# Optimization experiments

Hardware: AMD Instinct MI355X
Metric: run time of the kernel (lower is better)

Reference implementation:

```python
import jax, jax.numpy as jnp
import numpy as np

B = 4096
P_HID = 1024
H_HID = 512
MAX_P = 128
MAX_HE = MAX_P // 3  # 42
TAU = 1.0
EPS = 1e-20


def setup_inputs() -> dict:
    key = jax.random.key(0)
    ks = jax.random.split(key, 12)
    s_p = 1.0 / np.sqrt(P_HID)
    s_h = 1.0 / np.sqrt(H_HID)
    # gumbel noise: g = -log(-log(U))
    u_p = jax.random.uniform(ks[3], (B, MAX_P, 2), minval=EPS, maxval=1.0)
    u_h = jax.random.uniform(ks[4], (B, MAX_HE, 2), minval=EPS, maxval=1.0)
    return {
        "particle_h": jax.random.normal(ks[0], (B, P_HID), jnp.float32),
        "edge_h": jax.random.normal(ks[1], (B, H_HID), jnp.float32),
        "hyperedge_h": jax.random.normal(ks[2], (B, H_HID), jnp.float32),
        "g_p": -jnp.log(-jnp.log(u_p)),
        "g_h": -jnp.log(-jnp.log(u_h)),
        "W1_p": jax.random.normal(ks[5], (P_HID, P_HID), jnp.float32) * s_p,
        "b1_p": jnp.zeros((P_HID,), jnp.float32),
        "W2_p": jax.random.normal(ks[6], (P_HID, MAX_P), jnp.float32) * s_p,
        "b2_p": jnp.zeros((MAX_P,), jnp.float32),
        "W1_h": jax.random.normal(ks[7], (H_HID, H_HID), jnp.float32) * s_h,
        "b1_h": jnp.zeros((H_HID,), jnp.float32),
        "W2_h": jax.random.normal(ks[8], (H_HID, MAX_HE), jnp.float32) * s_h,
        "b2_h": jnp.zeros((MAX_HE,), jnp.float32),
    }


def _gumbel_hard_st(logits, g, tau):
    """F.gumbel_softmax(stack([l,-l],-1), tau, hard=True)[...,0] (straight-through)."""
    y = jax.nn.softmax((jnp.stack([logits, -logits], axis=-1) + g) / tau, axis=-1)
    y0 = y[..., 0]
    hard0 = (y0 > y[..., 1]).astype(y0.dtype)
    return hard0 + y0 - jax.lax.stop_gradient(y0)


def _mlp(x, W1, b1, W2, b2):
    return jax.nn.gelu(x @ W1 + b1, approximate=False) @ W2 + b2


def reference(particle_h, edge_h, hyperedge_h, g_p, g_h,
              W1_p, b1_p, W2_p, b2_p, W1_h, b1_h, W2_h, b2_h):
    particle_logits = _mlp(particle_h, W1_p, b1_p, W2_p, b2_p)      # [B, MAX_P]
    particle_mask = _gumbel_hard_st(particle_logits, g_p, TAU)      # [B, MAX_P]
    n_particles = particle_mask.sum(axis=-1).astype(jnp.int32)      # [B]

    # Ragged edge lists as a fixed padded buffer: all C(MAX_P,2) lexicographic
    # pairs (same order as torch.combinations); pair (i,j), i<j, is valid for
    # batch b iff j < n_particles[b].
    ii, jj = jnp.triu_indices(MAX_P, k=1)
    edge_index = jnp.stack([ii, jj]).astype(jnp.int32)              # [2, E_max]
    edge_valid = jj[None, :] < n_particles[:, None]                 # [B, E_max] bool

    hyperedge_logits = _mlp(hyperedge_h, W1_h, b1_h, W2_h, b2_h)    # [B, MAX_HE]
    hyperedge_mask = _gumbel_hard_st(hyperedge_logits, g_h, TAU)
    n_hyperedges = hyperedge_mask.sum(axis=-1).astype(jnp.int32)

    return (particle_mask, n_particles, edge_index, edge_valid,
            hyperedge_mask, n_hyperedges)
```

## Files before the change

### kernel.cpp

```cpp
#include <hip/hip_runtime.h>
#include <hip/hip_bf16.h>
#include <math.h>

typedef __bf16 bf16_t;
typedef bf16_t bf16x8 __attribute__((ext_vector_type(8)));
typedef bf16_t bf16x4 __attribute__((ext_vector_type(4)));
typedef float f32x4 __attribute__((ext_vector_type(4)));
typedef unsigned int u32;

#define B_SZ 4096
#define P_HID 1024
#define H_HID 512
#define MAX_P 128
#define MAX_HE 42
#define HE_PAD 64
#define E_MAX 8128
#define E_MAX4 2032

__device__ __forceinline__ void async_cp16(const bf16_t* g, bf16_t* l) {
    __builtin_amdgcn_global_load_lds(
        (const __attribute__((address_space(1))) u32*)g,
        (__attribute__((address_space(3))) u32*)l, 16, 0, 0);
}

__device__ __forceinline__ float gelu_exact(float v) {
    return 0.5f * v * (1.f + erff(v * 0.70710678118654752f));
}

template<int BM, int BN, int MODE>
__global__ __launch_bounds__(256, 2) void gemm_sp(
    const bf16_t* __restrict__ Ahi, const bf16_t* __restrict__ Alo,
    const bf16_t* __restrict__ BThi, const bf16_t* __restrict__ BTlo,
    const float* __restrict__ bias,
    float* __restrict__ Cf, bf16_t* __restrict__ Chi, bf16_t* __restrict__ Clo,
    int M, int N, int K, int kchunk)
{
    constexpr int MT = BM / 32;
    constexpr int NT = BN / 32;
    constexpr int OPS_A = BM / 16;
    constexpr int OPS_B = BN / 16;
    constexpr int NOPS = 2 * OPS_A + 2 * OPS_B;

    __shared__ __align__(16) bf16_t smem[(2 * BM + 2 * BN) * 32];
    bf16_t* const As0 = smem;
    bf16_t* const As1 = smem + BM * 32;
    bf16_t* const Bs0 = smem + 2 * BM * 32;
    bf16_t* const Bs1 = smem + 2 * BM * 32 + BN * 32;

    const int tid  = threadIdx.x;
    const int lane = tid & 63;
    const int wid  = tid >> 6;
    const int wm   = wid & 1;
    const int wn   = wid >> 1;
    const int bm   = blockIdx.y * BM;
    const int bn   = blockIdx.x * BN;
    const int k0   = blockIdx.z * kchunk;

    const int srow = lane >> 2;
    const int scol = (lane & 3) * 8;

    f32x4 acc[MT][NT];
#pragma unroll
    for (int i = 0; i < MT; ++i)
#pragma unroll
        for (int j = 0; j < NT; ++j)
            acc[i][j] = (f32x4){0.f, 0.f, 0.f, 0.f};

    const bf16_t* const gA0 = Ahi  + (size_t)bm * K;
    const bf16_t* const gA1 = Alo  + (size_t)bm * K;
    const bf16_t* const gB0 = BThi + (size_t)bn * K;
    const bf16_t* const gB1 = BTlo + (size_t)bn * K;

    const int fr = lane & 15;
    const int fq = lane >> 4;

    for (int kt = k0; kt < k0 + kchunk; kt += 32) {
        __syncthreads();
#pragma unroll
        for (int o = 0; o < NOPS; ++o) {
            if ((o & 3) != wid) continue;
            const bf16_t* gsrc;
            bf16_t* lbase;
            int q;
            if (o < OPS_A)               { q = o;                 gsrc = gA0; lbase = As0; }
            else if (o < 2 * OPS_A)      { q = o - OPS_A;         gsrc = gA1; lbase = As1; }
            else if (o < 2 * OPS_A + OPS_B) { q = o - 2 * OPS_A;  gsrc = gB0; lbase = Bs0; }
            else                         { q = o - 2 * OPS_A - OPS_B; gsrc = gB1; lbase = Bs1; }
            async_cp16(gsrc + (size_t)(q * 16 + srow) * K + kt + scol,
                       lbase + q * 16 * 32);
        }
        __syncthreads();

        bf16x8 ah[MT], al[MT], bh[NT], bl[NT];
#pragma unroll
        for (int i = 0; i < MT; ++i) {
            const int row = wm * (BM / 2) + i * 16 + fr;
            ah[i] = *(const bf16x8*)(As0 + row * 32 + fq * 8);
            al[i] = *(const bf16x8*)(As1 + row * 32 + fq * 8);
        }
#pragma unroll
        for (int j = 0; j < NT; ++j) {
            const int row = wn * (BN / 2) + j * 16 + fr;
            bh[j] = *(const bf16x8*)(Bs0 + row * 32 + fq * 8);
            bl[j] = *(const bf16x8*)(Bs1 + row * 32 + fq * 8);
        }
#pragma unroll
        for (int i = 0; i < MT; ++i)
#pragma unroll
            for (int j = 0; j < NT; ++j) {
                acc[i][j] = __builtin_amdgcn_mfma_f32_16x16x32_bf16(ah[i], bh[j], acc[i][j], 0, 0, 0);
                acc[i][j] = __builtin_amdgcn_mfma_f32_16x16x32_bf16(ah[i], bl[j], acc[i][j], 0, 0, 0);
                acc[i][j] = __builtin_amdgcn_mfma_f32_16x16x32_bf16(al[i], bh[j], acc[i][j], 0, 0, 0);
            }
    }

#pragma unroll
    for (int i = 0; i < MT; ++i)
#pragma unroll
        for (int j = 0; j < NT; ++j) {
            const int col  = bn + wn * (BN / 2) + j * 16 + fr;
            const int row0 = bm + wm * (BM / 2) + i * 16 + fq * 4;
            if (MODE == 0) {
                const float bj = bias[col];
#pragma unroll
                for (int r = 0; r < 4; ++r) {
                    float v = gelu_exact(acc[i][j][r] + bj);
                    bf16_t h = (bf16_t)v;
                    bf16_t l = (bf16_t)(v - (float)h);
                    const size_t off = (size_t)(row0 + r) * N + col;
                    Chi[off] = h;
                    Clo[off] = l;
                }
            } else {
#pragma unroll
                for (int r = 0; r < 4; ++r)
                    atomicAdd(&Cf[(size_t)(row0 + r) * N + col], acc[i][j][r]);
            }
        }
}

__global__ __launch_bounds__(256) void split_rows(
    const float* __restrict__ x, bf16_t* __restrict__ hi, bf16_t* __restrict__ lo, int n4)
{
    int i = blockIdx.x * 256 + threadIdx.x;
    if (i >= n4) return;
    float4 v = ((const float4*)x)[i];
    float vv[4] = {v.x, v.y, v.z, v.w};
    bf16x4 h, l;
#pragma unroll
    for (int r = 0; r < 4; ++r) {
        bf16_t hh = (bf16_t)vv[r];
        h[r] = hh;
        l[r] = (bf16_t)(vv[r] - (float)hh);
    }
    ((bf16x4*)hi)[i] = h;
    ((bf16x4*)lo)[i] = l;
}

__global__ __launch_bounds__(256) void wsplit_t(
    const float* __restrict__ W, bf16_t* __restrict__ Thi, bf16_t* __restrict__ Tlo,
    int K, int N)
{
    __shared__ float t[32][33];
    const int n0 = blockIdx.x * 32, k0 = blockIdx.y * 32;
    const int tx = threadIdx.x & 31, ty = threadIdx.x >> 5;
    for (int r = ty; r < 32; r += 8) {
        const int n = n0 + tx;
        t[r][tx] = (n < N) ? W[(size_t)(k0 + r) * N + n] : 0.f;
    }
    __syncthreads();
    for (int r = ty; r < 32; r += 8) {
        const float x = t[tx][r];
        bf16_t h = (bf16_t)x;
        bf16_t l = (bf16_t)(x - (float)h);
        const size_t off = (size_t)(n0 + r) * K + k0 + tx;
        Thi[off] = h;
        Tlo[off] = l;
    }
}

__global__ __launch_bounds__(256) void init_logits(
    const float* __restrict__ b2p, const float* __restrict__ b2h,
    float* __restrict__ logp, float* __restrict__ logh)
{
    const int i = blockIdx.x * 256 + threadIdx.x;
    const int NP = B_SZ * MAX_P;
    if (i < NP) {
        logp[i] = b2p[i & (MAX_P - 1)];
    } else {
        const int r = i - NP;
        if (r < B_SZ * HE_PAD) {
            const int c = r & (HE_PAD - 1);
            logh[r] = (c < MAX_HE) ? b2h[c] : 0.f;
        }
    }
}

__global__ __launch_bounds__(64) void mask_count(
    const float* __restrict__ logits, const float* __restrict__ g,
    float* __restrict__ out_mask, float* __restrict__ out_n,
    int* __restrict__ ws_n, int L, int ls)
{
    const int b = blockIdx.x;
    const int t = threadIdx.x;
    float cnt = 0.f;
    for (int i = t; i < L; i += 64) {
        const float l  = logits[(size_t)b * ls + i];
        const float g0 = g[((size_t)b * L + i) * 2 + 0];
        const float g1 = g[((size_t)b * L + i) * 2 + 1];
        const float hard = ((l + g0) > (g1 - l)) ? 1.f : 0.f;
        out_mask[(size_t)b * L + i] = hard;
        cnt += hard;
    }
#pragma unroll
    for (int off = 32; off > 0; off >>= 1) cnt += __shfl_down(cnt, off, 64);
    if (t == 0) {
        out_n[b] = cnt;
        if (ws_n) ws_n[b] = (int)cnt;
    }
}

__device__ __forceinline__ int tri_off(int i) { return (i * (255 - i)) >> 1; }

__global__ __launch_bounds__(256) void edge_index_kernel(
    float* __restrict__ out_ei, int* __restrict__ ws_jj)
{
    int e = blockIdx.x * 256 + threadIdx.x;
    if (e >= E_MAX) return;
    int i = (int)((255.0 - sqrt(65025.0 - 8.0 * (double)e)) * 0.5);
    if (i < 0) i = 0;
    if (i > 126) i = 126;
    while (i > 0 && tri_off(i) > e) --i;
    while (i < 126 && tri_off(i + 1) <= e) ++i;
    int j = i + 1 + (e - tri_off(i));
    out_ei[e] = (float)i;
    out_ei[E_MAX + e] = (float)j;
    ws_jj[e] = j;
}

__global__ __launch_bounds__(256) void edge_valid_kernel(
    const int* __restrict__ ws_jj, const int* __restrict__ ws_n,
    float* __restrict__ out, int total4)
{
    int idx = blockIdx.x * 256 + threadIdx.x;
    if (idx >= total4) return;
    int b = idx / E_MAX4;
    int q = idx - b * E_MAX4;
    int4 j4 = ((const int4*)ws_jj)[q];
    int n = ws_n[b];
    float4 v;
    v.x = (j4.x < n) ? 1.f : 0.f;
    v.y = (j4.y < n) ? 1.f : 0.f;
    v.z = (j4.z < n) ? 1.f : 0.f;
    v.w = (j4.w < n) ? 1.f : 0.f;
    ((float4*)out)[idx] = v;
}

extern "C" void kernel_launch(void* const* d_in, const int* in_sizes, int n_in,
                              void* d_out, int out_size, void* d_ws, size_t ws_size,
                              hipStream_t stream)
{
    const float* particle_h  = (const float*)d_in[0];
    const float* hyperedge_h = (const float*)d_in[2];
    const float* g_p  = (const float*)d_in[3];
    const float* g_h  = (const float*)d_in[4];
    const float* W1_p = (const float*)d_in[5];
    const float* b1_p = (const float*)d_in[6];
    const float* W2_p = (const float*)d_in[7];
    const float* b2_p = (const float*)d_in[8];
    const float* W1_h = (const float*)d_in[9];
    const float* b1_h = (const float*)d_in[10];
    const float* W2_h = (const float*)d_in[11];
    const float* b2_h = (const float*)d_in[12];

    float* out = (float*)d_out;
    float* out_pmask = out;
    float* out_np    = out_pmask + (size_t)B_SZ * MAX_P;
    float* out_ei    = out_np + B_SZ;
    float* out_ev    = out_ei + 2 * E_MAX;
    float* out_hmask = out_ev + (size_t)B_SZ * E_MAX;
    float* out_nh    = out_hmask + (size_t)B_SZ * MAX_HE;

    char* w = (char*)d_ws;
    bf16_t* pA_hi  = (bf16_t*)w;                    w += (size_t)B_SZ * P_HID * 2;
    bf16_t* pA_lo  = (bf16_t*)w;                    w += (size_t)B_SZ * P_HID * 2;
    bf16_t* hA_hi  = (bf16_t*)w;                    w += (size_t)B_SZ * H_HID * 2;
    bf16_t* hA_lo  = (bf16_t*)w;                    w += (size_t)B_SZ * H_HID * 2;
    bf16_t* hidp_hi = (bf16_t*)w;                   w += (size_t)B_SZ * P_HID * 2;
    bf16_t* hidp_lo = (bf16_t*)w;                   w += (size_t)B_SZ * P_HID * 2;
    bf16_t* hidh_hi = (bf16_t*)w;                   w += (size_t)B_SZ * H_HID * 2;
    bf16_t* hidh_lo = (bf16_t*)w;                   w += (size_t)B_SZ * H_HID * 2;
    bf16_t* W1pT_hi = (bf16_t*)w;                   w += (size_t)P_HID * P_HID * 2;
    bf16_t* W1pT_lo = (bf16_t*)w;                   w += (size_t)P_HID * P_HID * 2;
    bf16_t* W2pT_hi = (bf16_t*)w;                   w += (size_t)MAX_P * P_HID * 2;
    bf16_t* W2pT_lo = (bf16_t*)w;                   w += (size_t)MAX_P * P_HID * 2;
    bf16_t* W1hT_hi = (bf16_t*)w;                   w += (size_t)H_HID * H_HID * 2;
    bf16_t* W1hT_lo = (bf16_t*)w;                   w += (size_t)H_HID * H_HID * 2;
    bf16_t* W2hT_hi = (bf16_t*)w;                   w += (size_t)HE_PAD * H_HID * 2;
    bf16_t* W2hT_lo = (bf16_t*)w;                   w += (size_t)HE_PAD * H_HID * 2;
    float*  log_p   = (float*)w;                    w += (size_t)B_SZ * MAX_P * 4;
    float*  log_h   = (float*)w;                    w += (size_t)B_SZ * HE_PAD * 4;
    int*    ws_np   = (int*)w;                      w += B_SZ * 4;
    int*    ws_jj   = (int*)w;

    split_rows<<<(B_SZ * P_HID / 4 + 255) / 256, 256, 0, stream>>>(
        particle_h, pA_hi, pA_lo, B_SZ * P_HID / 4);
    split_rows<<<(B_SZ * H_HID / 4 + 255) / 256, 256, 0, stream>>>(
        hyperedge_h, hA_hi, hA_lo, B_SZ * H_HID / 4);
    wsplit_t<<<dim3(P_HID / 32, P_HID / 32), 256, 0, stream>>>(W1_p, W1pT_hi, W1pT_lo, P_HID, P_HID);
    wsplit_t<<<dim3(MAX_P / 32, P_HID / 32), 256, 0, stream>>>(W2_p, W2pT_hi, W2pT_lo, P_HID, MAX_P);
    wsplit_t<<<dim3(H_HID / 32, H_HID / 32), 256, 0, stream>>>(W1_h, W1hT_hi, W1hT_lo, H_HID, H_HID);
    wsplit_t<<<dim3(HE_PAD / 32, H_HID / 32), 256, 0, stream>>>(W2_h, W2hT_hi, W2hT_lo, H_HID, MAX_HE);
    init_logits<<<(B_SZ * (MAX_P + HE_PAD) + 255) / 256, 256, 0, stream>>>(
        b2_p, b2_h, log_p, log_h);

    gemm_sp<64, 128, 0><<<dim3(P_HID / 128, B_SZ / 64, 1), 256, 0, stream>>>(
        pA_hi, pA_lo, W1pT_hi, W1pT_lo, b1_p, nullptr, hidp_hi, hidp_lo,
        B_SZ, P_HID, P_HID, P_HID);
    gemm_sp<64, 128, 1><<<dim3(1, B_SZ / 64, 4), 256, 0, stream>>>(
        hidp_hi, hidp_lo, W2pT_hi, W2pT_lo, nullptr, log_p, nullptr, nullptr,
        B_SZ, MAX_P, P_HID, P_HID / 4);
    mask_count<<<B_SZ, 64, 0, stream>>>(log_p, g_p, out_pmask, out_np, ws_np, MAX_P, MAX_P);

    gemm_sp<64, 64, 0><<<dim3(H_HID / 64, B_SZ / 64, 1), 256, 0, stream>>>(
        hA_hi, hA_lo, W1hT_hi, W1hT_lo, b1_h, nullptr, hidh_hi, hidh_lo,
        B_SZ, H_HID, H_HID, H_HID);
    gemm_sp<64, 64, 1><<<dim3(1, B_SZ / 64, 4), 256, 0, stream>>>(
        hidh_hi, hidh_lo, W2hT_hi, W2hT_lo, nullptr, log_h, nullptr, nullptr,
        B_SZ, HE_PAD, H_HID, H_HID / 4);
    mask_count<<<B_SZ, 64, 0, stream>>>(log_h, g_h, out_hmask, out_nh, nullptr, MAX_HE, HE_PAD);

    edge_index_kernel<<<(E_MAX + 255) / 256, 256, 0, stream>>>(out_ei, ws_jj);
    edge_valid_kernel<<<(B_SZ * E_MAX4 + 255) / 256, 256, 0, stream>>>(
        ws_jj, ws_np, out_ev, B_SZ * E_MAX4);
}
```

Measured before the change: 311.8 us.

## Fuse prep kernels, fold mask/count into second GEMM, drop split-K atomics

All preprocessing (activation hi/lo splits, weight transposes, edge index, count zeroing) is merged into one launch. The second-layer GEMM loses split-K and its float atomics, and now computes bias, the Gumbel hard mask and per-row counts in its epilogue, which removes the logits buffer, the init kernel and the mask_count kernels. The hyperedge first-layer GEMM switches to 64x128 tiles. The cost is fewer blocks for the second GEMM (no K split), so it may leave the GPU underfilled.

```diff
diff --git a/kernel.cpp b/kernel.cpp
--- a/kernel.cpp
+++ b/kernel.cpp
@@ -4,7 +4,6 @@
 
 typedef __bf16 bf16_t;
 typedef bf16_t bf16x8 __attribute__((ext_vector_type(8)));
-typedef bf16_t bf16x4 __attribute__((ext_vector_type(4)));
 typedef float f32x4 __attribute__((ext_vector_type(4)));
 typedef unsigned int u32;
 
@@ -27,13 +26,13 @@
     return 0.5f * v * (1.f + erff(v * 0.70710678118654752f));
 }
 
-template<int BM, int BN, int MODE>
-__global__ __launch_bounds__(256, 2) void gemm_sp(
+template<int BM, int BN>
+__global__ __launch_bounds__(256, 2) void gemm1_gelu(
     const bf16_t* __restrict__ Ahi, const bf16_t* __restrict__ Alo,
     const bf16_t* __restrict__ BThi, const bf16_t* __restrict__ BTlo,
     const float* __restrict__ bias,
-    float* __restrict__ Cf, bf16_t* __restrict__ Chi, bf16_t* __restrict__ Clo,
-    int M, int N, int K, int kchunk)
+    bf16_t* __restrict__ Chi, bf16_t* __restrict__ Clo,
+    int N, int K)
 {
     constexpr int MT = BM / 32;
     constexpr int NT = BN / 32;
@@ -54,7 +53,6 @@
     const int wn   = wid >> 1;
     const int bm   = blockIdx.y * BM;
     const int bn   = blockIdx.x * BN;
-    const int k0   = blockIdx.z * kchunk;
 
     const int srow = lane >> 2;
     const int scol = (lane & 3) * 8;
@@ -74,7 +72,7 @@
     const int fr = lane & 15;
     const int fq = lane >> 4;
 
-    for (int kt = k0; kt < k0 + kchunk; kt += 32) {
+    for (int kt = 0; kt < K; kt += 32) {
         __syncthreads();
 #pragma unroll
         for (int o = 0; o < NOPS; ++o) {
@@ -82,10 +80,10 @@
             const bf16_t* gsrc;
             bf16_t* lbase;
             int q;
-            if (o < OPS_A)               { q = o;                 gsrc = gA0; lbase = As0; }
-            else if (o < 2 * OPS_A)      { q = o - OPS_A;         gsrc = gA1; lbase = As1; }
-            else if (o < 2 * OPS_A + OPS_B) { q = o - 2 * OPS_A;  gsrc = gB0; lbase = Bs0; }
-            else                         { q = o - 2 * OPS_A - OPS_B; gsrc = gB1; lbase = Bs1; }
+            if (o < OPS_A)                  { q = o;                     gsrc = gA0; lbase = As0; }
+            else if (o < 2 * OPS_A)         { q = o - OPS_A;             gsrc = gA1; lbase = As1; }
+            else if (o < 2 * OPS_A + OPS_B) { q = o - 2 * OPS_A;         gsrc = gB0; lbase = Bs0; }
+            else                            { q = o - 2 * OPS_A - OPS_B; gsrc = gB1; lbase = Bs1; }
             async_cp16(gsrc + (size_t)(q * 16 + srow) * K + kt + scol,
                        lbase + q * 16 * 32);
         }
@@ -120,30 +118,146 @@
         for (int j = 0; j < NT; ++j) {
             const int col  = bn + wn * (BN / 2) + j * 16 + fr;
             const int row0 = bm + wm * (BM / 2) + i * 16 + fq * 4;
-            if (MODE == 0) {
-                const float bj = bias[col];
-#pragma unroll
-                for (int r = 0; r < 4; ++r) {
-                    float v = gelu_exact(acc[i][j][r] + bj);
-                    bf16_t h = (bf16_t)v;
-                    bf16_t l = (bf16_t)(v - (float)h);
-                    const size_t off = (size_t)(row0 + r) * N + col;
-                    Chi[off] = h;
-                    Clo[off] = l;
+            const float bj = bias[col];
+#pragma unroll
+            for (int r = 0; r < 4; ++r) {
+                float v = gelu_exact(acc[i][j][r] + bj);
+                bf16_t h = (bf16_t)v;
+                bf16_t l = (bf16_t)(v - (float)h);
+                const size_t off = (size_t)(row0 + r) * N + col;
+                Chi[off] = h;
+                Clo[off] = l;
+            }
+        }
+}
+
+template<bool WNP>
+__global__ __launch_bounds__(256, 2) void gemm2_mask(
+    const bf16_t* __restrict__ Ahi, const bf16_t* __restrict__ Alo,
+    const bf16_t* __restrict__ BThi, const bf16_t* __restrict__ BTlo,
+    const float* __restrict__ bias, const float* __restrict__ g,
+    float* __restrict__ out_mask, float* __restrict__ out_n,
+    int* __restrict__ ws_n, int K, int NV)
+{
+    constexpr int BM = 64, BN = 64;
+    constexpr int MT = 2, NT = 2;
+    constexpr int OPS_A = 4, OPS_B = 4;
+    constexpr int NOPS = 16;
+
+    __shared__ __align__(16) bf16_t smem[(2 * BM + 2 * BN) * 32];
+    bf16_t* const As0 = smem;
+    bf16_t* const As1 = smem + BM * 32;
+    bf16_t* const Bs0 = smem + 2 * BM * 32;
+    bf16_t* const Bs1 = smem + 2 * BM * 32 + BN * 32;
+
+    const int tid  = threadIdx.x;
+    const int lane = tid & 63;
+    const int wid  = tid >> 6;
+    const int wm   = wid & 1;
+    const int wn   = wid >> 1;
+    const int bm   = blockIdx.y * BM;
+    const int bn   = blockIdx.x * BN;
+
+    const int srow = lane >> 2;
+    const int scol = (lane & 3) * 8;
+
+    f32x4 acc[MT][NT];
+#pragma unroll
+    for (int i = 0; i < MT; ++i)
+#pragma unroll
+        for (int j = 0; j < NT; ++j)
+            acc[i][j] = (f32x4){0.f, 0.f, 0.f, 0.f};
+
+    const bf16_t* const gA0 = Ahi  + (size_t)bm * K;
+    const bf16_t* const gA1 = Alo  + (size_t)bm * K;
+    const bf16_t* const gB0 = BThi + (size_t)bn * K;
+    const bf16_t* const gB1 = BTlo + (size_t)bn * K;
+
+    const int fr = lane & 15;
+    const int fq = lane >> 4;
+
+    for (int kt = 0; kt < K; kt += 32) {
+        __syncthreads();
+#pragma unroll
+        for (int o = 0; o < NOPS; ++o) {
+            if ((o & 3) != wid) continue;
+            const bf16_t* gsrc;
+            bf16_t* lbase;
+            int q;
+            if (o < OPS_A)                  { q = o;                     gsrc = gA0; lbase = As0; }
+            else if (o < 2 * OPS_A)         { q = o - OPS_A;             gsrc = gA1; lbase = As1; }
+            else if (o < 2 * OPS_A + OPS_B) { q = o - 2 * OPS_A;         gsrc = gB0; lbase = Bs0; }
+            else                            { q = o - 2 * OPS_A - OPS_B; gsrc = gB1; lbase = Bs1; }
+            async_cp16(gsrc + (size_t)(q * 16 + srow) * K + kt + scol,
+                       lbase + q * 16 * 32);
+        }
+        __syncthreads();
+
+        bf16x8 ah[MT], al[MT], bh[NT], bl[NT];
+#pragma unroll
+        for (int i = 0; i < MT; ++i) {
+            const int row = wm * 32 + i * 16 + fr;
+            ah[i] = *(const bf16x8*)(As0 + row * 32 + fq * 8);
+            al[i] = *(const bf16x8*)(As1 + row * 32 + fq * 8);
+        }
+#pragma unroll
+        for (int j = 0; j < NT; ++j) {
+            const int row = wn * 32 + j * 16 + fr;
+            bh[j] = *(const bf16x8*)(Bs0 + row * 32 + fq * 8);
+            bl[j] = *(const bf16x8*)(Bs1 + row * 32 + fq * 8);
+        }
+#pragma unroll
+        for (int i = 0; i < MT; ++i)
+#pragma unroll
+            for (int j = 0; j < NT; ++j) {
+                acc[i][j] = __builtin_amdgcn_mfma_f32_16x16x32_bf16(ah[i], bh[j], acc[i][j], 0, 0, 0);
+                acc[i][j] = __builtin_amdgcn_mfma_f32_16x16x32_bf16(ah[i], bl[j], acc[i][j], 0, 0, 0);
+                acc[i][j] = __builtin_amdgcn_mfma_f32_16x16x32_bf16(al[i], bh[j], acc[i][j], 0, 0, 0);
+            }
+    }
+
+#pragma unroll
+    for (int i = 0; i < MT; ++i) {
+#pragma unroll
+        for (int r = 0; r < 4; ++r) {
+            const int row = bm + wm * 32 + i * 16 + fq * 4 + r;
+            float s = 0.f;
+#pragma unroll
+            for (int j = 0; j < NT; ++j) {
+                const int col = bn + wn * 32 + j * 16 + fr;
+                if (col < NV) {
+                    const float v = acc[i][j][r] + bias[col];
+                    const size_t idx = (size_t)row * NV + col;
+                    const float g0 = g[2 * idx + 0];
+                    const float g1 = g[2 * idx + 1];
+                    const float m = ((v + g0) > (g1 - v)) ? 1.f : 0.f;
+                    out_mask[idx] = m;
+                    s += m;
                 }
-            } else {
-#pragma unroll
-                for (int r = 0; r < 4; ++r)
-                    atomicAdd(&Cf[(size_t)(row0 + r) * N + col], acc[i][j][r]);
             }
-        }
-}
-
-__global__ __launch_bounds__(256) void split_rows(
-    const float* __restrict__ x, bf16_t* __restrict__ hi, bf16_t* __restrict__ lo, int n4)
-{
-    int i = blockIdx.x * 256 + threadIdx.x;
-    if (i >= n4) return;
+            s += __shfl_xor(s, 1, 64);
+            s += __shfl_xor(s, 2, 64);
+            s += __shfl_xor(s, 4, 64);
+            s += __shfl_xor(s, 8, 64);
+            if (fr == 0) {
+                atomicAdd(&out_n[row], s);
+                if (WNP) atomicAdd(&ws_n[row], (int)s);
+            }
+        }
+    }
+}
+
+struct PrepArgs {
+    const float *ph, *hh, *W1p, *W2p, *W1h, *W2h;
+    bf16_t *pA_hi, *pA_lo, *hA_hi, *hA_lo;
+    bf16_t *W1pT_hi, *W1pT_lo, *W2pT_hi, *W2pT_lo;
+    bf16_t *W1hT_hi, *W1hT_lo, *W2hT_hi, *W2hT_lo;
+    float *out_ei; int *ws_jj;
+    float *out_np, *out_nh; int *ws_np;
+};
+
+__device__ __forceinline__ void split4(const float* x, bf16_t* hi, bf16_t* lo, int i) {
+    typedef bf16_t bf16x4 __attribute__((ext_vector_type(4)));
     float4 v = ((const float4*)x)[i];
     float vv[4] = {v.x, v.y, v.z, v.w};
     bf16x4 h, l;
@@ -157,20 +271,19 @@
     ((bf16x4*)lo)[i] = l;
 }
 
-__global__ __launch_bounds__(256) void wsplit_t(
-    const float* __restrict__ W, bf16_t* __restrict__ Thi, bf16_t* __restrict__ Tlo,
-    int K, int N)
-{
-    __shared__ float t[32][33];
-    const int n0 = blockIdx.x * 32, k0 = blockIdx.y * 32;
-    const int tx = threadIdx.x & 31, ty = threadIdx.x >> 5;
+__device__ __forceinline__ void tsplit(
+    const float* W, bf16_t* Thi, bf16_t* Tlo, int K, int N,
+    int t, int nx, float (*sh)[33], int tid)
+{
+    const int n0 = (t % nx) * 32, k0 = (t / nx) * 32;
+    const int tx = tid & 31, ty = tid >> 5;
     for (int r = ty; r < 32; r += 8) {
         const int n = n0 + tx;
-        t[r][tx] = (n < N) ? W[(size_t)(k0 + r) * N + n] : 0.f;
+        sh[r][tx] = (n < N) ? W[(size_t)(k0 + r) * N + n] : 0.f;
     }
     __syncthreads();
     for (int r = ty; r < 32; r += 8) {
-        const float x = t[tx][r];
+        const float x = sh[tx][r];
         bf16_t h = (bf16_t)x;
         bf16_t l = (bf16_t)(x - (float)h);
         const size_t off = (size_t)(n0 + r) * K + k0 + tx;
@@ -179,63 +292,48 @@
     }
 }
 
-__global__ __launch_bounds__(256) void init_logits(
-    const float* __restrict__ b2p, const float* __restrict__ b2h,
-    float* __restrict__ logp, float* __restrict__ logh)
-{
-    const int i = blockIdx.x * 256 + threadIdx.x;
-    const int NP = B_SZ * MAX_P;
-    if (i < NP) {
-        logp[i] = b2p[i & (MAX_P - 1)];
+__device__ __forceinline__ int tri_off(int i) { return (i * (255 - i)) >> 1; }
+
+__global__ __launch_bounds__(256) void prep_all(PrepArgs a)
+{
+    __shared__ float sh[32][33];
+    const int bid = blockIdx.x;
+    const int tid = threadIdx.x;
+
+    if (bid < 4096) {
+        split4(a.ph, a.pA_hi, a.pA_lo, bid * 256 + tid);
+    } else if (bid < 6144) {
+        split4(a.hh, a.hA_hi, a.hA_lo, (bid - 4096) * 256 + tid);
+    } else if (bid < 7168) {
+        tsplit(a.W1p, a.W1pT_hi, a.W1pT_lo, P_HID, P_HID, bid - 6144, 32, sh, tid);
+    } else if (bid < 7296) {
+        tsplit(a.W2p, a.W2pT_hi, a.W2pT_lo, P_HID, MAX_P, bid - 7168, 4, sh, tid);
+    } else if (bid < 7552) {
+        tsplit(a.W1h, a.W1hT_hi, a.W1hT_lo, H_HID, H_HID, bid - 7296, 16, sh, tid);
+    } else if (bid < 7584) {
+        tsplit(a.W2h, a.W2hT_hi, a.W2hT_lo, H_HID, MAX_HE, bid - 7552, 2, sh, tid);
+    } else if (bid < 7616) {
+        const int e = (bid - 7584) * 256 + tid;
+        if (e < E_MAX) {
+            int i = (int)((255.0 - sqrt(65025.0 - 8.0 * (double)e)) * 0.5);
+            if (i < 0) i = 0;
+            if (i > 126) i = 126;
+            while (i > 0 && tri_off(i) > e) --i;
+            while (i < 126 && tri_off(i + 1) <= e) ++i;
+            const int j = i + 1 + (e - tri_off(i));
+            a.out_ei[e] = (float)i;
+            a.out_ei[E_MAX + e] = (float)j;
+            a.ws_jj[e] = j;
+        }
     } else {
-        const int r = i - NP;
-        if (r < B_SZ * HE_PAD) {
-            const int c = r & (HE_PAD - 1);
-            logh[r] = (c < MAX_HE) ? b2h[c] : 0.f;
-        }
-    }
-}
-
-__global__ __launch_bounds__(64) void mask_count(
-    const float* __restrict__ logits, const float* __restrict__ g,
-    float* __restrict__ out_mask, float* __restrict__ out_n,
-    int* __restrict__ ws_n, int L, int ls)
-{
-    const int b = blockIdx.x;
-    const int t = threadIdx.x;
-    float cnt = 0.f;
-    for (int i = t; i < L; i += 64) {
-        const float l  = logits[(size_t)b * ls + i];
-        const float g0 = g[((size_t)b * L + i) * 2 + 0];
-        const float g1 = g[((size_t)b * L + i) * 2 + 1];
-        const float hard = ((l + g0) > (g1 - l)) ? 1.f : 0.f;
-        out_mask[(size_t)b * L + i] = hard;
-        cnt += hard;
-    }
-#pragma unroll
-    for (int off = 32; off > 0; off >>= 1) cnt += __shfl_down(cnt, off, 64);
-    if (t == 0) {
-        out_n[b] = cnt;
-        if (ws_n) ws_n[b] = (int)cnt;
-    }
-}
-
-__device__ __forceinline__ int tri_off(int i) { return (i * (255 - i)) >> 1; }
-
-__global__ __launch_bounds__(256) void edge_index_kernel(
-    float* __restrict__ out_ei, int* __restrict__ ws_jj)
-{
-    int e = blockIdx.x * 256 + threadIdx.x;
-    if (e >= E_MAX) return;
-    int i = (int)((255.0 - sqrt(65025.0 - 8.0 * (double)e)) * 0.5);
-    if (i < 0) i = 0;
-    if (i > 126) i = 126;
-    while (i > 0 && tri_off(i) > e) --i;
-    while (i < 126 && tri_off(i + 1) <= e) ++i;
-    int j = i + 1 + (e - tri_off(i));
-    out_ei[e] = (float)i;
-    out_ei[E_MAX + e] = (float)j;
-    ws_jj[e] = j;
+        const int gi = (bid - 7616) * 256 + tid;
+        if (gi < B_SZ) {
+            a.out_np[gi] = 0.f;
+            a.ws_np[gi] = 0;
+        } else if (gi < 2 * B_SZ) {
+            a.out_nh[gi - B_SZ] = 0.f;
+        }
+    }
 }
 
 __global__ __launch_bounds__(256) void edge_valid_kernel(
@@ -282,55 +380,49 @@
     float* out_nh    = out_hmask + (size_t)B_SZ * MAX_HE;
 
     char* w = (char*)d_ws;
-    bf16_t* pA_hi  = (bf16_t*)w;                    w += (size_t)B_SZ * P_HID * 2;
-    bf16_t* pA_lo  = (bf16_t*)w;                    w += (size_t)B_SZ * P_HID * 2;
-    bf16_t* hA_hi  = (bf16_t*)w;                    w += (size_t)B_SZ * H_HID * 2;
-    bf16_t* hA_lo  = (bf16_t*)w;                    w += (size_t)B_SZ * H_HID * 2;
-    bf16_t* hidp_hi = (bf16_t*)w;                   w += (size_t)B_SZ * P_HID * 2;
-    bf16_t* hidp_lo = (bf16_t*)w;                   w += (size_t)B_SZ * P_HID * 2;
-    bf16_t* hidh_hi = (bf16_t*)w;                   w += (size_t)B_SZ * H_HID * 2;
-    bf16_t* hidh_lo = (bf16_t*)w;                   w += (size_t)B_SZ * H_HID * 2;
-    bf16_t* W1pT_hi = (bf16_t*)w;                   w += (size_t)P_HID * P_HID * 2;
-    bf16_t* W1pT_lo = (bf16_t*)w;                   w += (size_t)P_HID * P_HID * 2;
-    bf16_t* W2pT_hi = (bf16_t*)w;                   w += (size_t)MAX_P * P_HID * 2;
-    bf16_t* W2pT_lo = (bf16_t*)w;                   w += (size_t)MAX_P * P_HID * 2;
-    bf16_t* W1hT_hi = (bf16_t*)w;                   w += (size_t)H_HID * H_HID * 2;
-    bf16_t* W1hT_lo = (bf16_t*)w;                   w += (size_t)H_HID * H_HID * 2;
-    bf16_t* W2hT_hi = (bf16_t*)w;                   w += (size_t)HE_PAD * H_HID * 2;
-    bf16_t* W2hT_lo = (bf16_t*)w;                   w += (size_t)HE_PAD * H_HID * 2;
-    float*  log_p   = (float*)w;                    w += (size_t)B_SZ * MAX_P * 4;
-    float*  log_h   = (float*)w;                    w += (size_t)B_SZ * HE_PAD * 4;
-    int*    ws_np   = (int*)w;                      w += B_SZ * 4;
+    bf16_t* pA_hi   = (bf16_t*)w;  w += (size_t)B_SZ * P_HID * 2;
+    bf16_t* pA_lo   = (bf16_t*)w;  w += (size_t)B_SZ * P_HID * 2;
+    bf16_t* hA_hi   = (bf16_t*)w;  w += (size_t)B_SZ * H_HID * 2;
+    bf16_t* hA_lo   = (bf16_t*)w;  w += (size_t)B_SZ * H_HID * 2;
+    bf16_t* hidp_hi = (bf16_t*)w;  w += (size_t)B_SZ * P_HID * 2;
+    bf16_t* hidp_lo = (bf16_t*)w;  w += (size_t)B_SZ * P_HID * 2;
+    bf16_t* hidh_hi = (bf16_t*)w;  w += (size_t)B_SZ * H_HID * 2;
+    bf16_t* hidh_lo = (bf16_t*)w;  w += (size_t)B_SZ * H_HID * 2;
+    bf16_t* W1pT_hi = (bf16_t*)w;  w += (size_t)P_HID * P_HID * 2;
+    bf16_t* W1pT_lo = (bf16_t*)w;  w += (size_t)P_HID * P_HID * 2;
+    bf16_t* W2pT_hi = (bf16_t*)w;  w += (size_t)MAX_P * P_HID * 2;
+    bf16_t* W2pT_lo = (bf16_t*)w;  w += (size_t)MAX_P * P_HID * 2;
+    bf16_t* W1hT_hi = (bf16_t*)w;  w += (size_t)H_HID * H_HID * 2;
+    bf16_t* W1hT_lo = (bf16_t*)w;  w += (size_t)H_HID * H_HID * 2;
+    bf16_t* W2hT_hi = (bf16_t*)w;  w += (size_t)HE_PAD * H_HID * 2;
+    bf16_t* W2hT_lo = (bf16_t*)w;  w += (size_t)HE_PAD * H_HID * 2;
+    int*    ws_np   = (int*)w;     w += B_SZ * 4;
     int*    ws_jj   = (int*)w;
 
-    split_rows<<<(B_SZ * P_HID / 4 + 255) / 256, 256, 0, stream>>>(
-        particle_h, pA_hi, pA_lo, B_SZ * P_HID / 4);
-    split_rows<<<(B_SZ * H_HID / 4 + 255) / 256, 256, 0, stream>>>(
-        hyperedge_h, hA_hi, hA_lo, B_SZ * H_HID / 4);
-    wsplit_t<<<dim3(P_HID / 32, P_HID / 32), 256, 0, stream>>>(W1_p, W1pT_hi, W1pT_lo, P_HID, P_HID);
-    wsplit_t<<<dim3(MAX_P / 32, P_HID / 32), 256, 0, stream>>>(W2_p, W2pT_hi, W2pT_lo, P_HID, MAX_P);
-    wsplit_t<<<dim3(H_HID / 32, H_HID / 32), 256, 0, stream>>>(W1_h, W1hT_hi, W1hT_lo, H_HID, H_HID);
-    wsplit_t<<<dim3(HE_PAD / 32, H_HID / 32), 256, 0, stream>>>(W2_h, W2hT_hi, W2hT_lo, H_HID, MAX_HE);
-    init_logits<<<(B_SZ * (MAX_P + HE_PAD) + 255) / 256, 256, 0, stream>>>(
-        b2_p, b2_h, log_p, log_h);
-
-    gemm_sp<64, 128, 0><<<dim3(P_HID / 128, B_SZ / 64, 1), 256, 0, stream>>>(
-        pA_hi, pA_lo, W1pT_hi, W1pT_lo, b1_p, nullptr, hidp_hi, hidp_lo,
-        B_SZ, P_HID, P_HID, P_HID);
-    gemm_sp<64, 128, 1><<<dim3(1, B_SZ / 64, 4), 256, 0, stream>>>(
-        hidp_hi, hidp_lo, W2pT_hi, W2pT_lo, nullptr, log_p, nullptr, nullptr,
-        B_SZ, MAX_P, P_HID, P_HID / 4);
-    mask_count<<<B_SZ, 64, 0, stream>>>(log_p, g_p, out_pmask, out_np, ws_np, MAX_P, MAX_P);
-
-    gemm_sp<64, 64, 0><<<dim3(H_HID / 64, B_SZ / 64, 1), 256, 0, stream>>>(
-        hA_hi, hA_lo, W1hT_hi, W1hT_lo, b1_h, nullptr, hidh_hi, hidh_lo,
-        B_SZ, H_HID, H_HID, H_HID);
-    gemm_sp<64, 64, 1><<<dim3(1, B_SZ / 64, 4), 256, 0, stream>>>(
-        hidh_hi, hidh_lo, W2hT_hi, W2hT_lo, nullptr, log_h, nullptr, nullptr,
-        B_SZ, HE_PAD, H_HID, H_HID / 4);
-    mask_count<<<B_SZ, 64, 0, stream>>>(log_h, g_h, out_hmask, out_nh, nullptr, MAX_HE, HE_PAD);
-
-    edge_index_kernel<<<(E_MAX + 255) / 256, 256, 0, stream>>>(out_ei, ws_jj);
+    PrepArgs pa;
+    pa.ph = particle_h; pa.hh = hyperedge_h;
+    pa.W1p = W1_p; pa.W2p = W2_p; pa.W1h = W1_h; pa.W2h = W2_h;
+    pa.pA_hi = pA_hi; pa.pA_lo = pA_lo; pa.hA_hi = hA_hi; pa.hA_lo = hA_lo;
+    pa.W1pT_hi = W1pT_hi; pa.W1pT_lo = W1pT_lo;
+    pa.W2pT_hi = W2pT_hi; pa.W2pT_lo = W2pT_lo;
+    pa.W1hT_hi = W1hT_hi; pa.W1hT_lo = W1hT_lo;
+    pa.W2hT_hi = W2hT_hi; pa.W2hT_lo = W2hT_lo;
+    pa.out_ei = out_ei; pa.ws_jj = ws_jj;
+    pa.out_np = out_np; pa.out_nh = out_nh; pa.ws_np = ws_np;
+    prep_all<<<7664, 256, 0, stream>>>(pa);
+
+    gemm1_gelu<64, 128><<<dim3(P_HID / 128, B_SZ / 64), 256, 0, stream>>>(
+        pA_hi, pA_lo, W1pT_hi, W1pT_lo, b1_p, hidp_hi, hidp_lo, P_HID, P_HID);
+    gemm1_gelu<64, 128><<<dim3(H_HID / 128, B_SZ / 64), 256, 0, stream>>>(
+        hA_hi, hA_lo, W1hT_hi, W1hT_lo, b1_h, hidh_hi, hidh_lo, H_HID, H_HID);
+
+    gemm2_mask<true><<<dim3(MAX_P / 64, B_SZ / 64), 256, 0, stream>>>(
+        hidp_hi, hidp_lo, W2pT_hi, W2pT_lo, b2_p, g_p,
+        out_pmask, out_np, ws_np, P_HID, MAX_P);
+    gemm2_mask<false><<<dim3(1, B_SZ / 64), 256, 0, stream>>>(
+        hidh_hi, hidh_lo, W2hT_hi, W2hT_lo, b2_h, g_h,
+        out_hmask, out_nh, nullptr, H_HID, MAX_HE);
+
     edge_valid_kernel<<<(B_SZ * E_MAX4 + 255) / 256, 256, 0, stream>>>(
         ws_jj, ws_np, out_ev, B_SZ * E_MAX4);
 }
```

After: 312.8 us. Within noise of the previous version (+0.3%).
